# Optimization experiments

Measured on AMD Instinct MI355X. Metric: run time of the kernel, lower is better.

The kernel has to match this reference:

```python
import jax, jax.numpy as jnp
import numpy as np

N_NODES = 50000
N_EDGES = 800000
N_RELS = 16
D = 128


def _rgcn_layer(h, W, b, loop_w, gate_w, src, dst, rel, norm, apply_relu, n_nodes):
    # Transform all node features by every relation weight once: [R, N, D_out].
    # Equivalent to DGL bmm_maybe_select's per-edge W[rel] bmm, but avoids an
    # [E, D, D] gather of weights.
    h_all = jnp.einsum('nd,rde->rne', h, W)
    msg = h_all[rel, src]                                    # [E, D_out]
    msg = msg * norm                                         # edge norm scaling
    gate_logit = jnp.einsum('nd,rd->rn', h, gate_w[..., 0])  # [R, N]
    gate = jax.nn.sigmoid(gate_logit[rel, src])[:, None]     # [E, 1]
    msg = msg * gate
    agg = jax.ops.segment_sum(msg, dst, num_segments=n_nodes)  # fn.sum -> dst
    out = agg + b + h @ loop_w                               # bias + self loop
    if apply_relu:
        out = jax.nn.relu(out)
    return out  # dropout is identity in eval mode


def setup_inputs() -> dict:
    key = jax.random.key(0)
    ks = jax.random.split(key, 12)
    gain = float(np.sqrt(2.0))  # relu gain (xavier-ish scale; values arbitrary)
    def xav(k, shape):
        fan = shape[-2] + shape[-1]
        s = gain * np.sqrt(6.0 / fan)
        return jax.random.uniform(k, shape, jnp.float32, -s, s)
    return {
        'h': jax.random.normal(ks[0], (N_NODES, D), jnp.float32),
        'norm': jax.random.uniform(ks[1], (N_EDGES, 1), jnp.float32),
        'weight0': xav(ks[2], (N_RELS, D, D)),
        'bias0': jnp.zeros((D,), jnp.float32),
        'loop_w0': xav(ks[3], (D, D)),
        'gate_w0': xav(ks[4], (N_RELS, D, 1)),
        'weight1': xav(ks[5], (N_RELS, D, D)),
        'bias1': jnp.zeros((D,), jnp.float32),
        'loop_w1': xav(ks[6], (D, D)),
        'gate_w1': xav(ks[7], (N_RELS, D, 1)),
        'src': jax.random.randint(ks[8], (N_EDGES,), 0, N_NODES, jnp.int32),
        'dst': jax.random.randint(ks[9], (N_EDGES,), 0, N_NODES, jnp.int32),
        'rel_type': jax.random.randint(ks[10], (N_EDGES,), 0, N_RELS, jnp.int32),
    }


def reference(h, norm, weight0, bias0, loop_w0, gate_w0,
              weight1, bias1, loop_w1, gate_w1, src, dst, rel_type):
    n_nodes = h.shape[0]
    # Layer 0: activation=relu (idx < num_hidden_layers - 1)
    h = _rgcn_layer(h, weight0, bias0, loop_w0, gate_w0, src, dst, rel_type,
                    norm, True, n_nodes)
    # Layer 1: no activation
    h = _rgcn_layer(h, weight1, bias1, loop_w1, gate_w1, src, dst, rel_type,
                    norm, False, n_nodes)
    return h
```

## Files before the change

### kernel.cpp

```cpp
#include <hip/hip_runtime.h>
#include <hip/hip_bf16.h>
#include <stdint.h>

#define NN 50000
#define NE 800000
#define NR 16
#define NP (NN * NR)
#define NB1 ((NP + 255) / 256)
#define TN 64
#define NT64 ((NN + TN - 1) / TN)

typedef unsigned short u16;
typedef unsigned int u32;

typedef __bf16 bf16x8 __attribute__((ext_vector_type(8)));
typedef __bf16 bf16x2 __attribute__((ext_vector_type(2)));
typedef float f32x4 __attribute__((ext_vector_type(4)));

__device__ __forceinline__ u16 f2bf(float f) {
  u32 u = __float_as_uint(f);
  u = u + 0x7FFFu + ((u >> 16) & 1u);
  return (u16)(u >> 16);
}

__device__ __forceinline__ u32 pk2bf(float x, float y) {
#if __has_builtin(__builtin_amdgcn_cvt_pk_bf16_f32)
  bf16x2 r = __builtin_amdgcn_cvt_pk_bf16_f32(x, y);
  union { bf16x2 v; u32 u; } c;
  c.v = r;
  return c.u;
#else
  return (u32)f2bf(x) | ((u32)f2bf(y) << 16);
#endif
}

__device__ __forceinline__ float bflo(u32 w) { return __uint_as_float(w << 16); }
__device__ __forceinline__ float bfhi(u32 w) { return __uint_as_float(w & 0xFFFF0000u); }

__global__ void hist_kernel(const int* __restrict__ dst, const int* __restrict__ rel,
                            int* __restrict__ counts) {
  int e = blockIdx.x * 256 + threadIdx.x;
  if (e < NE) atomicAdd(&counts[rel[e] * NN + dst[e]], 1);
}

__global__ void scan_partial(const int* __restrict__ counts, int* __restrict__ bsum) {
  __shared__ int buf[256];
  int t = threadIdx.x;
  int i = blockIdx.x * 256 + t;
  int v = (i < NP) ? counts[i] : 0;
  buf[t] = v;
  __syncthreads();
  for (int off = 1; off < 256; off <<= 1) {
    int x = buf[t];
    int y = (t >= off) ? buf[t - off] : 0;
    __syncthreads();
    buf[t] = x + y;
    __syncthreads();
  }
  if (t == 255) bsum[blockIdx.x] = buf[255];
}

__global__ void scan_mid(const int* __restrict__ bsum, int* __restrict__ boff,
                         int* __restrict__ total_out) {
  __shared__ int buf[1024];
  int t = threadIdx.x;
  int v[4];
  int sum = 0;
#pragma unroll
  for (int i = 0; i < 4; ++i) {
    int idx = t * 4 + i;
    v[i] = (idx < NB1) ? bsum[idx] : 0;
    sum += v[i];
  }
  buf[t] = sum;
  __syncthreads();
  for (int off = 1; off < 1024; off <<= 1) {
    int x = buf[t];
    int y = (t >= off) ? buf[t - off] : 0;
    __syncthreads();
    buf[t] = x + y;
    __syncthreads();
  }
  int excl = buf[t] - sum;
#pragma unroll
  for (int i = 0; i < 4; ++i) {
    int idx = t * 4 + i;
    if (idx < NB1) { boff[idx] = excl; excl += v[i]; }
  }
  if (t == 1023) *total_out = buf[1023];
}

__global__ void scan_final(const int* __restrict__ counts, const int* __restrict__ boff,
                           int* __restrict__ starts, int* __restrict__ cursor) {
  __shared__ int buf[256];
  int t = threadIdx.x;
  int i = blockIdx.x * 256 + t;
  int v = (i < NP) ? counts[i] : 0;
  buf[t] = v;
  __syncthreads();
  for (int off = 1; off < 256; off <<= 1) {
    int x = buf[t];
    int y = (t >= off) ? buf[t - off] : 0;
    __syncthreads();
    buf[t] = x + y;
    __syncthreads();
  }
  int s = boff[blockIdx.x] + buf[t] - v;
  if (i < NP) {
    starts[i] = s;
    cursor[i] = s;
  }
}

__global__ void scatter_kernel(const int* __restrict__ src, const int* __restrict__ dst,
                               const int* __restrict__ rel, const float* __restrict__ norm,
                               int* __restrict__ cursor, uint2* __restrict__ esd) {
  int e = blockIdx.x * 256 + threadIdx.x;
  if (e < NE) {
    int d = dst[e];
    int pos = atomicAdd(&cursor[rel[e] * NN + d], 1);
    esd[pos] = make_uint2(((u32)d << 16) | (u32)src[e], __float_as_uint(norm[e]));
  }
}

__global__ void convert_wt(const float* __restrict__ w0, const float* __restrict__ lw0,
                           const float* __restrict__ w1, const float* __restrict__ lw1,
                           u16* __restrict__ Wt) {
  int m = blockIdx.y;
  int idx = blockIdx.x * 256 + threadIdx.x;
  int d = idx >> 7, k = idx & 127;
  const float* s;
  if (m < 16) s = w0 + (size_t)m * 16384;
  else if (m == 16) s = lw0;
  else if (m < 33) s = w1 + (size_t)(m - 17) * 16384;
  else s = lw1;
  Wt[(size_t)m * 16384 + idx] = f2bf(s[k * 128 + d]);
}

__global__ void hconv_kernel(const float* __restrict__ h, u16* __restrict__ hbf) {
  int i = blockIdx.x * 256 + threadIdx.x;
  float4 v = ((const float4*)h)[i];
  ushort4 u;
  u.x = f2bf(v.x); u.y = f2bf(v.y); u.z = f2bf(v.z); u.w = f2bf(v.w);
  ((ushort4*)hbf)[i] = u;
}

__global__ void gates_kernel(const u16* __restrict__ hbf, const float* __restrict__ gw,
                             float* __restrict__ gates) {
  __shared__ float hs[16 * 132];
  __shared__ float gws[16 * 132];
  int t = threadIdx.x;
  int n0 = blockIdx.x * 16;
#pragma unroll
  for (int i = 0; i < 2; ++i) {
    int f = t + 256 * i;
    int row = f >> 5, c4 = (f & 31) * 4;
    ushort4 u = *(const ushort4*)&hbf[(size_t)(n0 + row) * 128 + c4];
    hs[row * 132 + c4 + 0] = __uint_as_float((u32)u.x << 16);
    hs[row * 132 + c4 + 1] = __uint_as_float((u32)u.y << 16);
    hs[row * 132 + c4 + 2] = __uint_as_float((u32)u.z << 16);
    hs[row * 132 + c4 + 3] = __uint_as_float((u32)u.w << 16);
    *(float4*)&gws[row * 132 + c4] = *(const float4*)&gw[row * 128 + c4];
  }
  __syncthreads();
  int nl = t >> 4, r = t & 15;
  float s = 0.f;
#pragma unroll 8
  for (int k = 0; k < 128; ++k) s += hs[nl * 132 + k] * gws[r * 132 + k];
  gates[r * NN + n0 + nl] = 1.f / (1.f + __expf(-s));
}

template <int LAYER>
__global__ __launch_bounds__(256, 4)
void fused_kernel(const u16* __restrict__ hbf, const uint2* __restrict__ esd,
                  const float* __restrict__ gates, const int* __restrict__ starts,
                  const u16* __restrict__ Wt, const float* __restrict__ bias,
                  u16* __restrict__ hb_out, float* __restrict__ fout) {
  __shared__ u16 As[2][TN * 136];
  const u32* hbf32 = (const u32*)hbf;
  int t = threadIdx.x;
  int n0 = blockIdx.x * TN;
  int wave = t >> 6, lane = t & 63;
  int wd = wave * 32;
  int mrow = lane & 15, quad = lane >> 4;
  int vb = n0 + wave * 16;
  int ve = vb + 16;
  if (ve > NN) ve = NN;
  bool aggok = vb < NN;

  f32x4 acc[2][4];
#pragma unroll
  for (int i = 0; i < 2; ++i)
#pragma unroll
    for (int j = 0; j < 4; ++j) acc[i][j] = (f32x4){0.f, 0.f, 0.f, 0.f};

  bf16x8 fw[4][2];

#define LOAD_FW(MAT)                                                          \
  {                                                                           \
    const u16* wmat = Wt + (size_t)(MAT) * 16384;                             \
    _Pragma("unroll")                                                         \
    for (int kk = 0; kk < 4; ++kk)                                            \
      _Pragma("unroll")                                                       \
      for (int i2 = 0; i2 < 2; ++i2)                                          \
        fw[kk][i2] = *(const bf16x8*)&wmat[(wd + i2 * 16 + mrow) * 128 +      \
                                           kk * 32 + quad * 8];               \
  }

#define DO_AGG(R, B, S, E)                                                    \
  {                                                                           \
    u32* asp = (u32*)(&As[B][0]) + (wave * 16) * 68 + lane;                   \
    const float* gp = gates + (size_t)(R) * NN;                               \
    float a0 = 0.f, a1 = 0.f;                                                 \
    int cur = 0;                                                              \
    int j = (S);                                                              \
    for (; j + 8 <= (E); j += 8) {                                            \
      uint2 p[8];                                                             \
      _Pragma("unroll")                                                       \
      for (int i = 0; i < 8; ++i) p[i] = esd[j + i];                          \
      u32 w[8];                                                               \
      float gt[8];                                                            \
      _Pragma("unroll")                                                       \
      for (int i = 0; i < 8; ++i) {                                           \
        u32 sn = p[i].x & 0xFFFFu;                                            \
        w[i] = hbf32[sn * 64u + (u32)lane];                                   \
        gt[i] = gp[sn];                                                       \
      }                                                                       \
      _Pragma("unroll")                                                       \
      for (int i = 0; i < 8; ++i) {                                           \
        int local = (int)(p[i].x >> 16) - vb;                                 \
        while (cur < local) {                                                 \
          asp[cur * 68] = pk2bf(a0, a1);                                      \
          a0 = 0.f; a1 = 0.f; ++cur;                                          \
        }                                                                     \
        float coef = gt[i] * __uint_as_float(p[i].y);                         \
        a0 = fmaf(coef, bflo(w[i]), a0);                                      \
        a1 = fmaf(coef, bfhi(w[i]), a1);                                      \
      }                                                                       \
    }                                                                         \
    for (; j < (E); ++j) {                                                    \
      uint2 p = esd[j];                                                       \
      u32 sn = p.x & 0xFFFFu;                                                 \
      int local = (int)(p.x >> 16) - vb;                                      \
      while (cur < local) {                                                   \
        asp[cur * 68] = pk2bf(a0, a1);                                        \
        a0 = 0.f; a1 = 0.f; ++cur;                                            \
      }                                                                       \
      float coef = gp[sn] * __uint_as_float(p.y);                             \
      u32 w1_ = hbf32[sn * 64u + (u32)lane];                                  \
      a0 = fmaf(coef, bflo(w1_), a0);                                         \
      a1 = fmaf(coef, bfhi(w1_), a1);                                         \
    }                                                                         \
    while (cur < 16) {                                                        \
      asp[cur * 68] = pk2bf(a0, a1);                                          \
      a0 = 0.f; a1 = 0.f; ++cur;                                              \
    }                                                                         \
  }

#define DO_MFMA(B)                                                            \
  _Pragma("unroll")                                                           \
  for (int kk = 0; kk < 4; ++kk) {                                            \
    int k0 = kk * 32 + quad * 8;                                              \
    bf16x8 fb[4];                                                             \
    _Pragma("unroll")                                                         \
    for (int j2 = 0; j2 < 4; ++j2)                                            \
      fb[j2] = *(const bf16x8*)&As[B][(j2 * 16 + mrow) * 136 + k0];           \
    _Pragma("unroll")                                                         \
    for (int i2 = 0; i2 < 2; ++i2)                                            \
      _Pragma("unroll")                                                       \
      for (int j2 = 0; j2 < 4; ++j2)                                          \
        acc[i2][j2] = __builtin_amdgcn_mfma_f32_16x16x32_bf16(                \
            fw[kk][i2], fb[j2], acc[i2][j2], 0, 0, 0);                        \
  }

  int sC = 0, eC = 0, sN = 0, eN = 0;
  if (aggok) { sC = starts[vb]; eC = starts[ve]; }
  LOAD_FW(0);
  if (aggok) { sN = starts[NN + vb]; eN = starts[NN + ve]; }
  DO_AGG(0, 0, sC, eC);
  __syncthreads();

  for (int m = 0; m < 17; ++m) {
    DO_MFMA(m & 1);
    if (m < 16) LOAD_FW(m + 1);
    if (m < 15) {
      int r = m + 1;
      sC = sN; eC = eN;
      if (aggok && r < 15) {
        sN = starts[(r + 1) * NN + vb];
        eN = starts[(r + 1) * NN + ve];
      }
      DO_AGG(r, (m + 1) & 1, sC, eC);
      __syncthreads();
    } else if (m == 15) {
#pragma unroll
      for (int i = 0; i < 4; ++i) {
        int u8 = t + 256 * i;
        int row = u8 >> 4, c8 = (u8 & 15) * 8;
        int n = n0 + row;
        int nc = n < NN ? n : NN - 1;
        *(uint4*)&As[0][row * 136 + c8] = *(const uint4*)&hbf[(size_t)nc * 128 + c8];
      }
      __syncthreads();
    }
  }

  float4 bvv[2];
#pragma unroll
  for (int i2 = 0; i2 < 2; ++i2)
    bvv[i2] = *(const float4*)&bias[wd + i2 * 16 + quad * 4];
#pragma unroll
  for (int j2 = 0; j2 < 4; ++j2) {
    int n = n0 + j2 * 16 + mrow;
    if (n < NN) {
#pragma unroll
      for (int i2 = 0; i2 < 2; ++i2) {
        int d0 = wd + i2 * 16 + quad * 4;
        float v0 = acc[i2][j2][0] + bvv[i2].x;
        float v1 = acc[i2][j2][1] + bvv[i2].y;
        float v2 = acc[i2][j2][2] + bvv[i2].z;
        float v3 = acc[i2][j2][3] + bvv[i2].w;
        if (LAYER == 0) {
          v0 = fmaxf(v0, 0.f); v1 = fmaxf(v1, 0.f);
          v2 = fmaxf(v2, 0.f); v3 = fmaxf(v3, 0.f);
          uint2 st;
          st.x = pk2bf(v0, v1);
          st.y = pk2bf(v2, v3);
          *(uint2*)&hb_out[(size_t)n * 128 + d0] = st;
        } else {
          float4 st = make_float4(v0, v1, v2, v3);
          *(float4*)&fout[(size_t)n * 128 + d0] = st;
        }
      }
    }
  }
#undef LOAD_FW
#undef DO_AGG
#undef DO_MFMA
}

extern "C" void kernel_launch(void* const* d_in, const int* in_sizes, int n_in,
                              void* d_out, int out_size, void* d_ws, size_t ws_size,
                              hipStream_t stream) {
  const float* h0   = (const float*)d_in[0];
  const float* norm = (const float*)d_in[1];
  const float* w0   = (const float*)d_in[2];
  const float* b0   = (const float*)d_in[3];
  const float* lw0  = (const float*)d_in[4];
  const float* gw0  = (const float*)d_in[5];
  const float* w1   = (const float*)d_in[6];
  const float* b1   = (const float*)d_in[7];
  const float* lw1  = (const float*)d_in[8];
  const float* gw1  = (const float*)d_in[9];
  const int*   src  = (const int*)d_in[10];
  const int*   dst  = (const int*)d_in[11];
  const int*   rel  = (const int*)d_in[12];
  float* out = (float*)d_out;

  char* p = (char*)d_ws;
  auto alloc = [&](size_t bytes) -> void* {
    void* q = (void*)p;
    p += (bytes + 255) & ~(size_t)255;
    return q;
  };
  u16*   Wt     = (u16*)alloc((size_t)34 * 16384 * 2);
  float* gates  = (float*)alloc((size_t)NR * NN * 4);
  u16*   hbf0   = (u16*)alloc((size_t)NN * 128 * 2);
  u16*   hbf1   = (u16*)alloc((size_t)NN * 128 * 2);
  int*   counts = (int*)alloc((size_t)NP * 4);
  int*   cursor = (int*)alloc((size_t)NP * 4);
  int*   starts = (int*)alloc((size_t)(NP + 1) * 4);
  int*   bsum   = (int*)alloc((size_t)NB1 * 4);
  int*   boff   = (int*)alloc((size_t)NB1 * 4);
  uint2* esd    = (uint2*)alloc((size_t)NE * 8);

  hipMemsetAsync(counts, 0, (size_t)NP * 4, stream);
  hist_kernel<<<NE / 256, 256, 0, stream>>>(dst, rel, counts);
  scan_partial<<<NB1, 256, 0, stream>>>(counts, bsum);
  scan_mid<<<1, 1024, 0, stream>>>(bsum, boff, starts + NP);
  scan_final<<<NB1, 256, 0, stream>>>(counts, boff, starts, cursor);
  scatter_kernel<<<NE / 256, 256, 0, stream>>>(src, dst, rel, norm, cursor, esd);
  convert_wt<<<dim3(64, 34), 256, 0, stream>>>(w0, lw0, w1, lw1, Wt);
  hconv_kernel<<<NN * 32 / 256, 256, 0, stream>>>(h0, hbf0);

  gates_kernel<<<NN / 16, 256, 0, stream>>>(hbf0, gw0, gates);
  fused_kernel<0><<<NT64, 256, 0, stream>>>(hbf0, esd, gates, starts, Wt, b0,
                                            hbf1, nullptr);

  gates_kernel<<<NN / 16, 256, 0, stream>>>(hbf1, gw1, gates);
  fused_kernel<1><<<NT64, 256, 0, stream>>>(hbf1, esd, gates, starts,
                                            Wt + (size_t)17 * 16384, b1,
                                            nullptr, out);
}
```

Before: 528.8 us.

## Precompute per-edge coefficients and halve node tile to 32 per block

```diff
diff --git a/kernel.cpp b/kernel.cpp
--- a/kernel.cpp
+++ b/kernel.cpp
@@ -7,11 +7,13 @@
 #define NR 16
 #define NP (NN * NR)
 #define NB1 ((NP + 255) / 256)
-#define TN 64
-#define NT64 ((NN + TN - 1) / TN)
+#define TN 32
+#define NW 8
+#define NT32 ((NN + TN - 1) / TN)
 
 typedef unsigned short u16;
 typedef unsigned int u32;
+typedef unsigned char u8;
 
 typedef __bf16 bf16x8 __attribute__((ext_vector_type(8)));
 typedef __bf16 bf16x2 __attribute__((ext_vector_type(2)));
@@ -114,12 +116,16 @@
 
 __global__ void scatter_kernel(const int* __restrict__ src, const int* __restrict__ dst,
                                const int* __restrict__ rel, const float* __restrict__ norm,
-                               int* __restrict__ cursor, uint2* __restrict__ esd) {
+                               int* __restrict__ cursor, u32* __restrict__ esd4,
+                               u8* __restrict__ rels, float* __restrict__ norm_s) {
   int e = blockIdx.x * 256 + threadIdx.x;
   if (e < NE) {
     int d = dst[e];
-    int pos = atomicAdd(&cursor[rel[e] * NN + d], 1);
-    esd[pos] = make_uint2(((u32)d << 16) | (u32)src[e], __float_as_uint(norm[e]));
+    int r = rel[e];
+    int pos = atomicAdd(&cursor[r * NN + d], 1);
+    esd4[pos] = ((u32)d << 16) | (u32)src[e];
+    rels[pos] = (u8)r;
+    norm_s[pos] = norm[e];
   }
 }
 
@@ -170,10 +176,21 @@
   gates[r * NN + n0 + nl] = 1.f / (1.f + __expf(-s));
 }
 
+__global__ void coef_kernel(const u32* __restrict__ esd4, const u8* __restrict__ rels,
+                            const float* __restrict__ norm_s,
+                            const float* __restrict__ gates, float* __restrict__ coef) {
+  int e = blockIdx.x * 256 + threadIdx.x;
+  if (e < NE) {
+    u32 sn = esd4[e] & 0xFFFFu;
+    int r = rels[e];
+    coef[e] = gates[(size_t)r * NN + sn] * norm_s[e];
+  }
+}
+
 template <int LAYER>
-__global__ __launch_bounds__(256, 4)
-void fused_kernel(const u16* __restrict__ hbf, const uint2* __restrict__ esd,
-                  const float* __restrict__ gates, const int* __restrict__ starts,
+__global__ __launch_bounds__(256, 5)
+void fused_kernel(const u16* __restrict__ hbf, const u32* __restrict__ esd4,
+                  const float* __restrict__ coef, const int* __restrict__ starts,
                   const u16* __restrict__ Wt, const float* __restrict__ bias,
                   u16* __restrict__ hb_out, float* __restrict__ fout) {
   __shared__ u16 As[2][TN * 136];
@@ -183,16 +200,16 @@
   int wave = t >> 6, lane = t & 63;
   int wd = wave * 32;
   int mrow = lane & 15, quad = lane >> 4;
-  int vb = n0 + wave * 16;
-  int ve = vb + 16;
+  int vb = n0 + wave * NW;
+  int ve = vb + NW;
   if (ve > NN) ve = NN;
   bool aggok = vb < NN;
 
-  f32x4 acc[2][4];
+  f32x4 acc[2][2];
 #pragma unroll
   for (int i = 0; i < 2; ++i)
 #pragma unroll
-    for (int j = 0; j < 4; ++j) acc[i][j] = (f32x4){0.f, 0.f, 0.f, 0.f};
+    for (int j = 0; j < 2; ++j) acc[i][j] = (f32x4){0.f, 0.f, 0.f, 0.f};
 
   bf16x8 fw[4][2];
 
@@ -207,51 +224,39 @@
                                            kk * 32 + quad * 8];               \
   }
 
-#define DO_AGG(R, B, S, E)                                                    \
+#define DO_AGG(B, S, E)                                                       \
   {                                                                           \
-    u32* asp = (u32*)(&As[B][0]) + (wave * 16) * 68 + lane;                   \
-    const float* gp = gates + (size_t)(R) * NN;                               \
+    u32* asp = (u32*)(&As[B][0]) + (wave * NW) * 68 + lane;                   \
     float a0 = 0.f, a1 = 0.f;                                                 \
     int cur = 0;                                                              \
-    int j = (S);                                                              \
-    for (; j + 8 <= (E); j += 8) {                                            \
-      uint2 p[8];                                                             \
-      _Pragma("unroll")                                                       \
-      for (int i = 0; i < 8; ++i) p[i] = esd[j + i];                          \
-      u32 w[8];                                                               \
-      float gt[8];                                                            \
+    for (int j = (S); j < (E); j += 8) {                                      \
+      u32 ds[8];                                                              \
+      float cf[8];                                                            \
       _Pragma("unroll")                                                       \
       for (int i = 0; i < 8; ++i) {                                           \
-        u32 sn = p[i].x & 0xFFFFu;                                            \
-        w[i] = hbf32[sn * 64u + (u32)lane];                                   \
-        gt[i] = gp[sn];                                                       \
+        int ii = j + i;                                                       \
+        ii = ii < (E) ? ii : (E) - 1;                                         \
+        ds[i] = esd4[ii];                                                     \
+        cf[i] = coef[ii];                                                     \
       }                                                                       \
+      u32 w[8];                                                               \
+      _Pragma("unroll")                                                       \
+      for (int i = 0; i < 8; ++i)                                             \
+        w[i] = hbf32[(ds[i] & 0xFFFFu) * 64u + (u32)lane];                    \
       _Pragma("unroll")                                                       \
       for (int i = 0; i < 8; ++i) {                                           \
-        int local = (int)(p[i].x >> 16) - vb;                                 \
-        while (cur < local) {                                                 \
-          asp[cur * 68] = pk2bf(a0, a1);                                      \
-          a0 = 0.f; a1 = 0.f; ++cur;                                          \
+        if (j + i < (E)) {                                                    \
+          int local = (int)(ds[i] >> 16) - vb;                                \
+          while (cur < local) {                                               \
+            asp[cur * 68] = pk2bf(a0, a1);                                    \
+            a0 = 0.f; a1 = 0.f; ++cur;                                        \
+          }                                                                   \
+          a0 = fmaf(cf[i], bflo(w[i]), a0);                                   \
+          a1 = fmaf(cf[i], bfhi(w[i]), a1);                                   \
         }                                                                     \
-        float coef = gt[i] * __uint_as_float(p[i].y);                         \
-        a0 = fmaf(coef, bflo(w[i]), a0);                                      \
-        a1 = fmaf(coef, bfhi(w[i]), a1);                                      \
       }                                                                       \
     }                                                                         \
-    for (; j < (E); ++j) {                                                    \
-      uint2 p = esd[j];                                                       \
-      u32 sn = p.x & 0xFFFFu;                                                 \
-      int local = (int)(p.x >> 16) - vb;                                      \
-      while (cur < local) {                                                   \
-        asp[cur * 68] = pk2bf(a0, a1);                                        \
-        a0 = 0.f; a1 = 0.f; ++cur;                                            \
-      }                                                                       \
-      float coef = gp[sn] * __uint_as_float(p.y);                             \
-      u32 w1_ = hbf32[sn * 64u + (u32)lane];                                  \
-      a0 = fmaf(coef, bflo(w1_), a0);                                         \
-      a1 = fmaf(coef, bfhi(w1_), a1);                                         \
-    }                                                                         \
-    while (cur < 16) {                                                        \
+    while (cur < NW) {                                                        \
       asp[cur * 68] = pk2bf(a0, a1);                                          \
       a0 = 0.f; a1 = 0.f; ++cur;                                              \
     }                                                                         \
@@ -261,14 +266,14 @@
   _Pragma("unroll")                                                           \
   for (int kk = 0; kk < 4; ++kk) {                                            \
     int k0 = kk * 32 + quad * 8;                                              \
-    bf16x8 fb[4];                                                             \
+    bf16x8 fb[2];                                                             \
     _Pragma("unroll")                                                         \
-    for (int j2 = 0; j2 < 4; ++j2)                                            \
+    for (int j2 = 0; j2 < 2; ++j2)                                            \
       fb[j2] = *(const bf16x8*)&As[B][(j2 * 16 + mrow) * 136 + k0];           \
     _Pragma("unroll")                                                         \
     for (int i2 = 0; i2 < 2; ++i2)                                            \
       _Pragma("unroll")                                                       \
-      for (int j2 = 0; j2 < 4; ++j2)                                          \
+      for (int j2 = 0; j2 < 2; ++j2)                                          \
         acc[i2][j2] = __builtin_amdgcn_mfma_f32_16x16x32_bf16(                \
             fw[kk][i2], fb[j2], acc[i2][j2], 0, 0, 0);                        \
   }
@@ -277,7 +282,7 @@
   if (aggok) { sC = starts[vb]; eC = starts[ve]; }
   LOAD_FW(0);
   if (aggok) { sN = starts[NN + vb]; eN = starts[NN + ve]; }
-  DO_AGG(0, 0, sC, eC);
+  DO_AGG(0, sC, eC);
   __syncthreads();
 
   for (int m = 0; m < 17; ++m) {
@@ -290,13 +295,13 @@
         sN = starts[(r + 1) * NN + vb];
         eN = starts[(r + 1) * NN + ve];
       }
-      DO_AGG(r, (m + 1) & 1, sC, eC);
+      DO_AGG((m + 1) & 1, sC, eC);
       __syncthreads();
     } else if (m == 15) {
 #pragma unroll
-      for (int i = 0; i < 4; ++i) {
-        int u8 = t + 256 * i;
-        int row = u8 >> 4, c8 = (u8 & 15) * 8;
+      for (int i = 0; i < 2; ++i) {
+        int u8i = t + 256 * i;
+        int row = u8i >> 4, c8 = (u8i & 15) * 8;
         int n = n0 + row;
         int nc = n < NN ? n : NN - 1;
         *(uint4*)&As[0][row * 136 + c8] = *(const uint4*)&hbf[(size_t)nc * 128 + c8];
@@ -310,7 +315,7 @@
   for (int i2 = 0; i2 < 2; ++i2)
     bvv[i2] = *(const float4*)&bias[wd + i2 * 16 + quad * 4];
 #pragma unroll
-  for (int j2 = 0; j2 < 4; ++j2) {
+  for (int j2 = 0; j2 < 2; ++j2) {
     int n = n0 + j2 * 16 + mrow;
     if (n < NN) {
 #pragma unroll
@@ -372,23 +377,29 @@
   int*   starts = (int*)alloc((size_t)(NP + 1) * 4);
   int*   bsum   = (int*)alloc((size_t)NB1 * 4);
   int*   boff   = (int*)alloc((size_t)NB1 * 4);
-  uint2* esd    = (uint2*)alloc((size_t)NE * 8);
+  u32*   esd4   = (u32*)alloc((size_t)NE * 4);
+  u8*    rels   = (u8*)alloc((size_t)NE);
+  float* norm_s = (float*)alloc((size_t)NE * 4);
+  float* coef   = (float*)alloc((size_t)NE * 4);
 
   hipMemsetAsync(counts, 0, (size_t)NP * 4, stream);
   hist_kernel<<<NE / 256, 256, 0, stream>>>(dst, rel, counts);
   scan_partial<<<NB1, 256, 0, stream>>>(counts, bsum);
   scan_mid<<<1, 1024, 0, stream>>>(bsum, boff, starts + NP);
   scan_final<<<NB1, 256, 0, stream>>>(counts, boff, starts, cursor);
-  scatter_kernel<<<NE / 256, 256, 0, stream>>>(src, dst, rel, norm, cursor, esd);
+  scatter_kernel<<<NE / 256, 256, 0, stream>>>(src, dst, rel, norm, cursor,
+                                               esd4, rels, norm_s);
   convert_wt<<<dim3(64, 34), 256, 0, stream>>>(w0, lw0, w1, lw1, Wt);
   hconv_kernel<<<NN * 32 / 256, 256, 0, stream>>>(h0, hbf0);
 
   gates_kernel<<<NN / 16, 256, 0, stream>>>(hbf0, gw0, gates);
-  fused_kernel<0><<<NT64, 256, 0, stream>>>(hbf0, esd, gates, starts, Wt, b0,
+  coef_kernel<<<(NE + 255) / 256, 256, 0, stream>>>(esd4, rels, norm_s, gates, coef);
+  fused_kernel<0><<<NT32, 256, 0, stream>>>(hbf0, esd4, coef, starts, Wt, b0,
                                             hbf1, nullptr);
 
   gates_kernel<<<NN / 16, 256, 0, stream>>>(hbf1, gw1, gates);
-  fused_kernel<1><<<NT64, 256, 0, stream>>>(hbf1, esd, gates, starts,
+  coef_kernel<<<(NE + 255) / 256, 256, 0, stream>>>(esd4, rels, norm_s, gates, coef);
+  fused_kernel<1><<<NT32, 256, 0, stream>>>(hbf1, esd4, coef, starts,
                                             Wt + (size_t)17 * 16384, b1,
                                             nullptr, out);
 }
```

Measured after the change: 688.8 us. 30.3% more time.
